# Kernel tuning notes

Hardware: AMD Instinct MI355X
Metric: run time of the kernel (lower is better)

The kernel has to match this reference:

```python
import jax, jax.numpy as jnp
import numpy as np

N = 1_000_000
D_IN = 128
D_OUT = 128
S = 8192  # num_samples


def setup_inputs() -> dict:
    key = jax.random.key(0)
    k1, k2, k3, k4 = jax.random.split(key, 4)
    element_embeddings = jax.random.normal(k1, (N, D_IN), dtype=jnp.float32)
    w_att = jax.random.normal(k2, (D_IN,), dtype=jnp.float32) * (1.0 / np.sqrt(D_IN))
    w_out = jax.random.normal(k3, (D_OUT, D_IN), dtype=jnp.float32) * (1.0 / np.sqrt(D_IN))
    element_to_sample_map = jax.random.randint(k4, (N,), 0, S, dtype=jnp.int32)
    return {
        "element_embeddings": element_embeddings,
        "w_att": w_att,
        "w_out": w_out,
        "element_to_sample_map": element_to_sample_map,
        "num_samples": S,
    }


def reference(element_embeddings, w_att, w_out, element_to_sample_map, num_samples):
    idx = element_to_sample_map
    # attention scores: Linear(D_in, 1, bias=False) -> [N]
    scores = element_embeddings @ w_att  # [N]
    # scatter log-softmax over segments (eps=0), numerically stable
    seg_max = jax.ops.segment_max(scores, idx, num_segments=num_samples)  # [S]
    shifted = scores - seg_max[idx]  # [N]
    seg_sumexp = jax.ops.segment_sum(jnp.exp(shifted), idx, num_segments=num_samples)  # [S]
    attention_probs = jnp.exp(shifted - jnp.log(seg_sumexp)[idx])  # [N]
    # output projection then weighted scatter-sum pooling
    projected = element_embeddings @ w_out.T  # [N, D_out]
    return jax.ops.segment_sum(projected * attention_probs[:, None], idx, num_segments=num_samples)  # [S, D_out]
```

## Files before the change

kernel.cpp:

```cpp
#include <hip/hip_runtime.h>
#include <math.h>

__global__ __launch_bounds__(256) void k_hist(const int* __restrict__ idx,
                                              int* __restrict__ counts, int n) {
    int i = blockIdx.x * 256 + threadIdx.x;
    if (i < n) atomicAdd(&counts[idx[i]], 1);
}

__global__ __launch_bounds__(1024) void k_scan(const int* __restrict__ counts,
                                               int* __restrict__ base,
                                               int* __restrict__ cursor, int S) {
    __shared__ int sh[1024];
    int t = threadIdx.x;
    int loc[8];
    int sum = 0;
#pragma unroll
    for (int j = 0; j < 8; ++j) {
        int g = t * 8 + j;
        loc[j] = sum;
        sum += (g < S) ? counts[g] : 0;
    }
    sh[t] = sum;
    __syncthreads();
    int total = sum;
    for (int off = 1; off < 1024; off <<= 1) {
        int v = (t >= off) ? sh[t - off] : 0;
        __syncthreads();
        sh[t] += v;
        __syncthreads();
    }
    int excl = sh[t] - total;
#pragma unroll
    for (int j = 0; j < 8; ++j) {
        int g = t * 8 + j;
        if (g < S) {
            int b = excl + loc[j];
            base[g] = b;
            cursor[g] = b;
        }
    }
}

__global__ __launch_bounds__(256) void k_scatter(const int* __restrict__ idx,
                                                 int* __restrict__ cursor,
                                                 int* __restrict__ order, int n) {
    int i = blockIdx.x * 256 + threadIdx.x;
    if (i < n) {
        int s = idx[i];
        int pos = atomicAdd(&cursor[s], 1);
        order[pos] = i;
    }
}

__global__ __launch_bounds__(256, 4) void k_pool(
        const float* __restrict__ emb, const float* __restrict__ w_att,
        const int* __restrict__ base, const int* __restrict__ counts,
        const int* __restrict__ order, float* __restrict__ pooled, int S) {
    int wave = (blockIdx.x << 2) | (threadIdx.x >> 6);
    int lane = threadIdx.x & 63;
    if (wave >= S) return;
    int g   = lane >> 4;
    int l16 = lane & 15;
    int b   = base[wave];
    int cnt = counts[wave];
    const float* wrow = w_att + 8 * l16;
    float4 wa0 = *reinterpret_cast<const float4*>(wrow);
    float4 wa1 = *reinterpret_cast<const float4*>(wrow + 4);
    float4 a0 = make_float4(0.f, 0.f, 0.f, 0.f);
    float4 a1 = make_float4(0.f, 0.f, 0.f, 0.f);
    float Z = 0.f;
    if (cnt > 0) {
        int nit = (cnt + 3) >> 2;
        int e = g;
        int i0 = order[b + (e < cnt ? e : cnt - 1)];
        const float* r = emb + (size_t)i0 * 128 + 8 * l16;
        float4 v0 = *reinterpret_cast<const float4*>(r);
        float4 v1 = *reinterpret_cast<const float4*>(r + 4);
        for (int it = 0; it < nit; ++it) {
            int en = e + 4;
            int inext = order[b + (en < cnt ? en : cnt - 1)];
            const float* rn = emb + (size_t)inext * 128 + 8 * l16;
            float4 n0 = *reinterpret_cast<const float4*>(rn);
            float4 n1 = *reinterpret_cast<const float4*>(rn + 4);
            float part = v0.x * wa0.x + v0.y * wa0.y + v0.z * wa0.z + v0.w * wa0.w
                       + v1.x * wa1.x + v1.y * wa1.y + v1.z * wa1.z + v1.w * wa1.w;
            part += __shfl_xor(part, 1);
            part += __shfl_xor(part, 2);
            part += __shfl_xor(part, 4);
            part += __shfl_xor(part, 8);
            float ex = (e < cnt) ? __expf(part) : 0.f;
            Z += ex;
            a0.x = fmaf(ex, v0.x, a0.x);
            a0.y = fmaf(ex, v0.y, a0.y);
            a0.z = fmaf(ex, v0.z, a0.z);
            a0.w = fmaf(ex, v0.w, a0.w);
            a1.x = fmaf(ex, v1.x, a1.x);
            a1.y = fmaf(ex, v1.y, a1.y);
            a1.z = fmaf(ex, v1.z, a1.z);
            a1.w = fmaf(ex, v1.w, a1.w);
            v0 = n0;
            v1 = n1;
            e = en;
        }
    }
#pragma unroll
    for (int m = 16; m <= 32; m <<= 1) {
        a0.x += __shfl_xor(a0.x, m);
        a0.y += __shfl_xor(a0.y, m);
        a0.z += __shfl_xor(a0.z, m);
        a0.w += __shfl_xor(a0.w, m);
        a1.x += __shfl_xor(a1.x, m);
        a1.y += __shfl_xor(a1.y, m);
        a1.z += __shfl_xor(a1.z, m);
        a1.w += __shfl_xor(a1.w, m);
        Z    += __shfl_xor(Z,    m);
    }
    float rn_ = (Z > 0.f) ? (1.0f / Z) : 0.f;
    if (g == 0) {
        float* o = pooled + (size_t)wave * 128 + 8 * l16;
        float4 o0 = make_float4(a0.x * rn_, a0.y * rn_, a0.z * rn_, a0.w * rn_);
        float4 o1 = make_float4(a1.x * rn_, a1.y * rn_, a1.z * rn_, a1.w * rn_);
        *reinterpret_cast<float4*>(o)     = o0;
        *reinterpret_cast<float4*>(o + 4) = o1;
    }
}

#define SPB 8
__global__ __launch_bounds__(256, 4) void k_proj(
        const float* __restrict__ w_out, float* __restrict__ io, int S) {
    __shared__ float wl[128][68];
    __shared__ float pl[2][64];
    int t = threadIdx.x;
    int d = t & 127;
    int h = t >> 7;
    int s0 = blockIdx.x * SPB;
    float acc[SPB / 2];
#pragma unroll
    for (int j = 0; j < SPB / 2; ++j) acc[j] = 0.f;

    for (int ph = 0; ph < 2; ++ph) {
        __syncthreads();
        for (int j = t; j < 2048; j += 256) {
            int r  = j >> 4;
            int c4 = j & 15;
            float4 wv = reinterpret_cast<const float4*>(w_out + (size_t)r * 128 + ph * 64)[c4];
            wl[r][c4 * 4 + 0] = wv.x;
            wl[r][c4 * 4 + 1] = wv.y;
            wl[r][c4 * 4 + 2] = wv.z;
            wl[r][c4 * 4 + 3] = wv.w;
        }
        __syncthreads();
#pragma unroll
        for (int g = 0; g < SPB; g += 2) {
            if (t < 128) {
                int hh = t >> 6, kk = t & 63;
                int ss = s0 + g + hh;
                pl[hh][kk] = (ss < S) ? io[(size_t)ss * 128 + ph * 64 + kk] : 0.f;
            }
            __syncthreads();
            float a = 0.f;
#pragma unroll
            for (int k4 = 0; k4 < 16; ++k4) {
                float4 wv = *reinterpret_cast<const float4*>(&wl[d][k4 * 4]);
                float4 pv = *reinterpret_cast<const float4*>(&pl[h][k4 * 4]);
                a = fmaf(wv.x, pv.x, a);
                a = fmaf(wv.y, pv.y, a);
                a = fmaf(wv.z, pv.z, a);
                a = fmaf(wv.w, pv.w, a);
            }
            acc[g >> 1] += a;
            __syncthreads();
        }
    }
#pragma unroll
    for (int g = 0; g < SPB; g += 2) {
        int s = s0 + g + h;
        if (s < S) io[(size_t)s * 128 + d] = acc[g >> 1];
    }
}

extern "C" void kernel_launch(void* const* d_in, const int* in_sizes, int n_in,
                              void* d_out, int out_size, void* d_ws, size_t ws_size,
                              hipStream_t stream) {
    const float* emb   = (const float*)d_in[0];
    const float* w_att = (const float*)d_in[1];
    const float* w_out = (const float*)d_in[2];
    const int*   idx   = (const int*)d_in[3];
    const int N = in_sizes[0] / 128;
    const int S = out_size / 128;

    char* ws = (char*)d_ws;
    int* counts = (int*)(ws + 0);
    int* base   = (int*)(ws + 32 * 1024);
    int* cursor = (int*)(ws + 64 * 1024);
    int* order  = (int*)(ws + 128 * 1024);
    float* out  = (float*)d_out;

    hipMemsetAsync(counts, 0, (size_t)S * sizeof(int), stream);
    k_hist   <<<(N + 255) / 256, 256, 0, stream>>>(idx, counts, N);
    k_scan   <<<1, 1024, 0, stream>>>(counts, base, cursor, S);
    k_scatter<<<(N + 255) / 256, 256, 0, stream>>>(idx, cursor, order, N);
    k_pool   <<<(S + 3) / 4, 256, 0, stream>>>(emb, w_att, base, counts, order, out, S);
    k_proj   <<<(S + SPB - 1) / SPB, 256, 0, stream>>>(w_out, out, S);
}
```

Baseline: 261.8 us.

## Use block-local shared-memory histograms for segment sort, prefetch order indices, batch projection loads

Replaces global-atomic histogram and scatter with 64 blocks that each build a shared-memory histogram over a contiguous chunk and reserve per-block offsets in global memory, so the scatter uses shared-memory atomics. The pool kernel prefetches the order index two steps ahead to shorten the dependent load chain. The projection kernel loads all eight pooled rows at once and drops the per-pair barriers. Only 64 blocks are used for the sort phases, which may underuse the GPU's compute units.

Result: slower. 298.5 us (+14.0%).

```diff
diff --git a/kernel.cpp b/kernel.cpp
--- a/kernel.cpp
+++ b/kernel.cpp
@@ -1,15 +1,29 @@
 #include <hip/hip_runtime.h>
 #include <math.h>
 
-__global__ __launch_bounds__(256) void k_hist(const int* __restrict__ idx,
-                                              int* __restrict__ counts, int n) {
-    int i = blockIdx.x * 256 + threadIdx.x;
-    if (i < n) atomicAdd(&counts[idx[i]], 1);
+#define NB 64
+
+__global__ __launch_bounds__(1024) void k_hist2(const int* __restrict__ idx,
+                                                int* __restrict__ counts,
+                                                int* __restrict__ rb,
+                                                int n, int S) {
+    __shared__ int lh[8192];
+    int t = threadIdx.x, b = blockIdx.x;
+    for (int s = t; s < S; s += 1024) lh[s] = 0;
+    __syncthreads();
+    int chunk = (n + NB - 1) / NB;
+    int lo = b * chunk;
+    int hi = min(n, lo + chunk);
+    for (int i = lo + t; i < hi; i += 1024) atomicAdd(&lh[idx[i]], 1);
+    __syncthreads();
+    for (int s = t; s < S; s += 1024) {
+        int h = lh[s];
+        rb[b * S + s] = (h > 0) ? atomicAdd(&counts[s], h) : 0;
+    }
 }
 
 __global__ __launch_bounds__(1024) void k_scan(const int* __restrict__ counts,
-                                               int* __restrict__ base,
-                                               int* __restrict__ cursor, int S) {
+                                               int* __restrict__ base, int S) {
     __shared__ int sh[1024];
     int t = threadIdx.x;
     int loc[8];
@@ -33,21 +47,25 @@
 #pragma unroll
     for (int j = 0; j < 8; ++j) {
         int g = t * 8 + j;
-        if (g < S) {
-            int b = excl + loc[j];
-            base[g] = b;
-            cursor[g] = b;
-        }
-    }
-}
-
-__global__ __launch_bounds__(256) void k_scatter(const int* __restrict__ idx,
-                                                 int* __restrict__ cursor,
-                                                 int* __restrict__ order, int n) {
-    int i = blockIdx.x * 256 + threadIdx.x;
-    if (i < n) {
+        if (g < S) base[g] = excl + loc[j];
+    }
+}
+
+__global__ __launch_bounds__(1024) void k_scatter2(const int* __restrict__ idx,
+                                                   const int* __restrict__ base,
+                                                   const int* __restrict__ rb,
+                                                   int* __restrict__ order,
+                                                   int n, int S) {
+    __shared__ int cur[8192];
+    int t = threadIdx.x, b = blockIdx.x;
+    for (int s = t; s < S; s += 1024) cur[s] = base[s] + rb[b * S + s];
+    __syncthreads();
+    int chunk = (n + NB - 1) / NB;
+    int lo = b * chunk;
+    int hi = min(n, lo + chunk);
+    for (int i = lo + t; i < hi; i += 1024) {
         int s = idx[i];
-        int pos = atomicAdd(&cursor[s], 1);
+        int pos = atomicAdd(&cur[s], 1);
         order[pos] = i;
     }
 }
@@ -70,25 +88,27 @@
     float4 a1 = make_float4(0.f, 0.f, 0.f, 0.f);
     float Z = 0.f;
     if (cnt > 0) {
-        int nit = (cnt + 3) >> 2;
+        const int* ob = order + b;
+        int last = cnt - 1;
         int e = g;
-        int i0 = order[b + (e < cnt ? e : cnt - 1)];
-        const float* r = emb + (size_t)i0 * 128 + 8 * l16;
+        int i_cur = ob[min(e, last)];
+        int i_nxt = ob[min(e + 4, last)];
+        const float* r = emb + (size_t)i_cur * 128 + 8 * l16;
         float4 v0 = *reinterpret_cast<const float4*>(r);
         float4 v1 = *reinterpret_cast<const float4*>(r + 4);
+        int nit = (cnt + 3) >> 2;
         for (int it = 0; it < nit; ++it) {
-            int en = e + 4;
-            int inext = order[b + (en < cnt ? en : cnt - 1)];
-            const float* rn = emb + (size_t)inext * 128 + 8 * l16;
+            const float* rn = emb + (size_t)i_nxt * 128 + 8 * l16;
             float4 n0 = *reinterpret_cast<const float4*>(rn);
             float4 n1 = *reinterpret_cast<const float4*>(rn + 4);
+            int i_n2 = ob[min(e + 8, last)];
             float part = v0.x * wa0.x + v0.y * wa0.y + v0.z * wa0.z + v0.w * wa0.w
                        + v1.x * wa1.x + v1.y * wa1.y + v1.z * wa1.z + v1.w * wa1.w;
             part += __shfl_xor(part, 1);
             part += __shfl_xor(part, 2);
             part += __shfl_xor(part, 4);
             part += __shfl_xor(part, 8);
-            float ex = (e < cnt) ? __expf(part) : 0.f;
+            float ex = (e <= last) ? __expf(part) : 0.f;
             Z += ex;
             a0.x = fmaf(ex, v0.x, a0.x);
             a0.y = fmaf(ex, v0.y, a0.y);
@@ -98,9 +118,7 @@
             a1.y = fmaf(ex, v1.y, a1.y);
             a1.z = fmaf(ex, v1.z, a1.z);
             a1.w = fmaf(ex, v1.w, a1.w);
-            v0 = n0;
-            v1 = n1;
-            e = en;
+            v0 = n0; v1 = n1; i_nxt = i_n2; e += 4;
         }
     }
 #pragma unroll
@@ -118,10 +136,8 @@
     float rn_ = (Z > 0.f) ? (1.0f / Z) : 0.f;
     if (g == 0) {
         float* o = pooled + (size_t)wave * 128 + 8 * l16;
-        float4 o0 = make_float4(a0.x * rn_, a0.y * rn_, a0.z * rn_, a0.w * rn_);
-        float4 o1 = make_float4(a1.x * rn_, a1.y * rn_, a1.z * rn_, a1.w * rn_);
-        *reinterpret_cast<float4*>(o)     = o0;
-        *reinterpret_cast<float4*>(o + 4) = o1;
+        *reinterpret_cast<float4*>(o)     = make_float4(a0.x * rn_, a0.y * rn_, a0.z * rn_, a0.w * rn_);
+        *reinterpret_cast<float4*>(o + 4) = make_float4(a1.x * rn_, a1.y * rn_, a1.z * rn_, a1.w * rn_);
     }
 }
 
@@ -129,53 +145,46 @@
 __global__ __launch_bounds__(256, 4) void k_proj(
         const float* __restrict__ w_out, float* __restrict__ io, int S) {
     __shared__ float wl[128][68];
-    __shared__ float pl[2][64];
+    __shared__ float pl[SPB][64];
     int t = threadIdx.x;
     int d = t & 127;
     int h = t >> 7;
     int s0 = blockIdx.x * SPB;
-    float acc[SPB / 2];
-#pragma unroll
-    for (int j = 0; j < SPB / 2; ++j) acc[j] = 0.f;
+    float acc[4] = {0.f, 0.f, 0.f, 0.f};
 
     for (int ph = 0; ph < 2; ++ph) {
         __syncthreads();
         for (int j = t; j < 2048; j += 256) {
-            int r  = j >> 4;
-            int c4 = j & 15;
+            int r = j >> 4, c4 = j & 15;
             float4 wv = reinterpret_cast<const float4*>(w_out + (size_t)r * 128 + ph * 64)[c4];
-            wl[r][c4 * 4 + 0] = wv.x;
-            wl[r][c4 * 4 + 1] = wv.y;
-            wl[r][c4 * 4 + 2] = wv.z;
-            wl[r][c4 * 4 + 3] = wv.w;
-        }
-        __syncthreads();
-#pragma unroll
-        for (int g = 0; g < SPB; g += 2) {
-            if (t < 128) {
-                int hh = t >> 6, kk = t & 63;
-                int ss = s0 + g + hh;
-                pl[hh][kk] = (ss < S) ? io[(size_t)ss * 128 + ph * 64 + kk] : 0.f;
+            *reinterpret_cast<float4*>(&wl[r][c4 * 4]) = wv;
+        }
+        if (t < 128) {
+            int sm = t >> 4, c4 = t & 15;
+            int ss = s0 + sm;
+            float4 pv = (ss < S)
+                ? reinterpret_cast<const float4*>(io + (size_t)ss * 128 + ph * 64)[c4]
+                : make_float4(0.f, 0.f, 0.f, 0.f);
+            *reinterpret_cast<float4*>(&pl[sm][c4 * 4]) = pv;
+        }
+        __syncthreads();
+#pragma unroll
+        for (int k4 = 0; k4 < 16; ++k4) {
+            float4 wv = *reinterpret_cast<const float4*>(&wl[d][k4 * 4]);
+#pragma unroll
+            for (int j = 0; j < 4; ++j) {
+                float4 pv = *reinterpret_cast<const float4*>(&pl[2 * j + h][k4 * 4]);
+                acc[j] = fmaf(wv.x, pv.x, acc[j]);
+                acc[j] = fmaf(wv.y, pv.y, acc[j]);
+                acc[j] = fmaf(wv.z, pv.z, acc[j]);
+                acc[j] = fmaf(wv.w, pv.w, acc[j]);
             }
-            __syncthreads();
-            float a = 0.f;
-#pragma unroll
-            for (int k4 = 0; k4 < 16; ++k4) {
-                float4 wv = *reinterpret_cast<const float4*>(&wl[d][k4 * 4]);
-                float4 pv = *reinterpret_cast<const float4*>(&pl[h][k4 * 4]);
-                a = fmaf(wv.x, pv.x, a);
-                a = fmaf(wv.y, pv.y, a);
-                a = fmaf(wv.z, pv.z, a);
-                a = fmaf(wv.w, pv.w, a);
-            }
-            acc[g >> 1] += a;
-            __syncthreads();
-        }
-    }
-#pragma unroll
-    for (int g = 0; g < SPB; g += 2) {
-        int s = s0 + g + h;
-        if (s < S) io[(size_t)s * 128 + d] = acc[g >> 1];
+        }
+    }
+#pragma unroll
+    for (int j = 0; j < 4; ++j) {
+        int s = s0 + 2 * j + h;
+        if (s < S) io[(size_t)s * 128 + d] = acc[j];
     }
 }
 
@@ -192,14 +201,14 @@
     char* ws = (char*)d_ws;
     int* counts = (int*)(ws + 0);
     int* base   = (int*)(ws + 32 * 1024);
-    int* cursor = (int*)(ws + 64 * 1024);
-    int* order  = (int*)(ws + 128 * 1024);
+    int* rb     = (int*)(ws + 128 * 1024);
+    int* order  = (int*)(ws + 128 * 1024 + (size_t)NB * 8192 * 4);
     float* out  = (float*)d_out;
 
     hipMemsetAsync(counts, 0, (size_t)S * sizeof(int), stream);
-    k_hist   <<<(N + 255) / 256, 256, 0, stream>>>(idx, counts, N);
-    k_scan   <<<1, 1024, 0, stream>>>(counts, base, cursor, S);
-    k_scatter<<<(N + 255) / 256, 256, 0, stream>>>(idx, cursor, order, N);
+    k_hist2  <<<NB, 1024, 0, stream>>>(idx, counts, rb, N, S);
+    k_scan   <<<1, 1024, 0, stream>>>(counts, base, S);
+    k_scatter2<<<NB, 1024, 0, stream>>>(idx, base, rb, order, N, S);
     k_pool   <<<(S + 3) / 4, 256, 0, stream>>>(emb, w_att, base, counts, order, out, S);
     k_proj   <<<(S + SPB - 1) / SPB, 256, 0, stream>>>(w_out, out, S);
 }
```
